# Kernel optimization log

Hardware: AMD Instinct MI355X
Metric: run time of the kernel (lower is better)

## Reference

```python
import jax, jax.numpy as jnp
import numpy as np

D_MODEL = 2048
D_FFN = 8192
RANK = 16
MOD_SCALE = 0.1
EPS = 1e-6


def setup_inputs() -> dict:
    key = jax.random.key(0)
    ks = jax.random.split(key, 8)
    B, S = 2, 2048
    init_scale = 0.01
    return {
        'hidden_states': jax.random.normal(ks[0], (B, S, D_MODEL), jnp.float32),
        'attn_output': jax.random.normal(ks[1], (B, S, D_MODEL), jnp.float32),
        'A': jax.random.normal(ks[2], (D_MODEL, RANK), jnp.float32) * (init_scale / np.sqrt(D_MODEL)),
        'Bmat': jax.random.normal(ks[3], (RANK, D_FFN), jnp.float32) * (init_scale / np.sqrt(RANK)),
        'W_in': jax.random.normal(ks[4], (D_FFN, D_MODEL), jnp.float32) * 0.02,  # gate_proj.weight
        'W_up': jax.random.normal(ks[5], (D_FFN, D_MODEL), jnp.float32) * 0.02,  # up_proj.weight
        'W_down': jax.random.normal(ks[6], (D_MODEL, D_FFN), jnp.float32) * 0.02,  # down_proj.weight
        'gamma': jnp.ones((D_MODEL,), jnp.float32),  # post_attention_layernorm (RMSNorm) weight
    }


def _rmsnorm(x, gamma):
    var = jnp.mean(x * x, axis=-1, keepdims=True)
    return x * jax.lax.rsqrt(var + EPS) * gamma


def reference(hidden_states, attn_output, A, Bmat, W_in, W_up, W_down, gamma):
    residual = hidden_states
    # Neuro-plastic modulation: [B,S,r]
    modulation = MOD_SCALE * jnp.tanh(jnp.einsum('bsd,dr->bsr', attn_output, A))
    # NPT applies post-attn norm to the residual (not residual+attn)
    h = _rmsnorm(residual, gamma)  # [B,S,d_model]
    # Fused per-token weight delta: delta_w^T @ h == B^T ((A^T h) * mod)
    hA = jnp.einsum('bsd,dr->bsr', h, A)  # [B,S,r]
    delta_out = jnp.einsum('bsr,rf->bsf', hA * modulation, Bmat)  # [B,S,d_ffn]
    gate = jax.nn.silu(jnp.einsum('bsd,fd->bsf', h, W_in) + delta_out)
    up = jnp.einsum('bsd,fd->bsf', h, W_up)
    out = jnp.einsum('bsf,df->bsd', gate * up, W_down)
    return residual + out
```

## Files before the change

### kernel.cpp

```cpp
#include <hip/hip_runtime.h>
#include <cstdint>
#include <cstddef>

#define D_MODEL 2048
#define D_FFN   8192
#define RANK    16
#define EPS     1e-6f
#define MOD_SCALE 0.1f

typedef float    f32x4 __attribute__((ext_vector_type(4)));
typedef _Float16 half8 __attribute__((ext_vector_type(8)));

__device__ __forceinline__ void async_load16(const void* g, void* l) {
  __builtin_amdgcn_global_load_lds(
      (const __attribute__((address_space(1))) uint32_t*)g,
      (__attribute__((address_space(3))) uint32_t*)l,
      16, 0, 0);
}

__device__ __forceinline__ void stage_round(const _Float16* __restrict__ g,
                                            size_t stride, _Float16* l, int tid) {
  const int row = tid >> 3;
  const int cs  = (tid & 7) ^ (row & 7);
  async_load16(g + (size_t)row * stride + (size_t)cs * 8, l + tid * 8);
}

__device__ __forceinline__ half8 frag64(const _Float16* base, int row, int ck) {
  return *(const half8*)&base[row * 64 + ((ck ^ (row & 7)) * 8)];
}

#define PRIO1() __builtin_amdgcn_s_setprio(1)
#define PRIO0() __builtin_amdgcn_s_setprio(0)
#define VMW(n)  asm volatile("s_waitcnt vmcnt(" #n ")" ::: "memory")
#define LKW(n)  asm volatile("s_waitcnt lgkmcnt(" #n ")" ::: "memory")
#define BARM()  asm volatile("s_barrier" ::: "memory")

__global__ __launch_bounds__(256) void convert3_f32_f16(
    const float* __restrict__ s0, const float* __restrict__ s1,
    const float* __restrict__ s2,
    _Float16* __restrict__ d0, _Float16* __restrict__ d1,
    _Float16* __restrict__ d2)
{
  const int w = blockIdx.x >> 13;
  const float*   s = (w == 0) ? s0 : (w == 1) ? s1 : s2;
  _Float16*      d = (w == 0) ? d0 : (w == 1) ? d1 : d2;
  size_t i = ((size_t)(blockIdx.x & 8191) * 256 + threadIdx.x) * 8;
  f32x4 a = *(const f32x4*)(s + i);
  f32x4 b = *(const f32x4*)(s + i + 4);
  half8 h;
  #pragma unroll
  for (int j = 0; j < 4; ++j) { h[j] = (_Float16)a[j]; h[4+j] = (_Float16)b[j]; }
  *(half8*)(d + i) = h;
}

__global__ __launch_bounds__(256) void convert_f32_f16(
    const float* __restrict__ s, _Float16* __restrict__ d)
{
  size_t i = ((size_t)blockIdx.x * 256 + threadIdx.x) * 8;
  f32x4 a = *(const f32x4*)(s + i);
  f32x4 b = *(const f32x4*)(s + i + 4);
  half8 h;
  #pragma unroll
  for (int j = 0; j < 4; ++j) { h[j] = (_Float16)a[j]; h[4+j] = (_Float16)b[j]; }
  *(half8*)(d + i) = h;
}

__global__ __launch_bounds__(256) void prep_kernel(
    const float* __restrict__ hs, const float* __restrict__ attn,
    const float* __restrict__ Amat, const float* __restrict__ gamma,
    _Float16* __restrict__ h16, float* __restrict__ cmat)
{
  const int token = blockIdx.x;
  const int tid   = threadIdx.x;
  const int lane  = tid & 63;
  const int wv    = tid >> 6;
  const size_t tb = (size_t)token * D_MODEL;
  const int base  = tid * 8;

  f32x4 x0 = *(const f32x4*)(hs + tb + base);
  f32x4 x1 = *(const f32x4*)(hs + tb + base + 4);
  f32x4 a0 = *(const f32x4*)(attn + tb + base);
  f32x4 a1 = *(const f32x4*)(attn + tb + base + 4);

  float ss = 0.f;
  #pragma unroll
  for (int j = 0; j < 4; ++j) ss += x0[j]*x0[j] + x1[j]*x1[j];
  #pragma unroll
  for (int off = 32; off > 0; off >>= 1) ss += __shfl_xor(ss, off, 64);

  __shared__ float red[4];
  __shared__ float redp[4][RANK];
  __shared__ float redh[4][RANK];
  if (lane == 0) red[wv] = ss;
  __syncthreads();
  const float tot = red[0] + red[1] + red[2] + red[3];
  const float rms = rsqrtf(tot * (1.0f / D_MODEL) + EPS);

  f32x4 g0 = *(const f32x4*)(gamma + base);
  f32x4 g1 = *(const f32x4*)(gamma + base + 4);
  float hv[8], av[8];
  #pragma unroll
  for (int j = 0; j < 4; ++j) {
    hv[j]   = x0[j] * rms * g0[j];
    hv[4+j] = x1[j] * rms * g1[j];
    av[j]   = a0[j];
    av[4+j] = a1[j];
  }
  half8 hh;
  #pragma unroll
  for (int j = 0; j < 8; ++j) hh[j] = (_Float16)hv[j];
  *(half8*)(h16 + tb + base) = hh;

  float pa[RANK], ph[RANK];
  #pragma unroll
  for (int r = 0; r < RANK; ++r) { pa[r] = 0.f; ph[r] = 0.f; }
  #pragma unroll
  for (int e = 0; e < 8; ++e) {
    const f32x4* Ar = (const f32x4*)(Amat + (size_t)(base + e) * RANK);
    #pragma unroll
    for (int q = 0; q < 4; ++q) {
      f32x4 ar = Ar[q];
      #pragma unroll
      for (int j = 0; j < 4; ++j) {
        pa[q*4+j] += av[e] * ar[j];
        ph[q*4+j] += hv[e] * ar[j];
      }
    }
  }
  #pragma unroll
  for (int r = 0; r < RANK; ++r) {
    #pragma unroll
    for (int off = 32; off > 0; off >>= 1) {
      pa[r] += __shfl_xor(pa[r], off, 64);
      ph[r] += __shfl_xor(ph[r], off, 64);
    }
  }
  if (lane == 0) {
    #pragma unroll
    for (int r = 0; r < RANK; ++r) { redp[wv][r] = pa[r]; redh[wv][r] = ph[r]; }
  }
  __syncthreads();
  if (tid < RANK) {
    float sp = redp[0][tid] + redp[1][tid] + redp[2][tid] + redp[3][tid];
    float sh = redh[0][tid] + redh[1][tid] + redh[2][tid] + redh[3][tid];
    cmat[(size_t)token * RANK + tid] = sh * (MOD_SCALE * tanhf(sp));
  }
}

__device__ __forceinline__ void rdA(half8 (&d)[4][2], const _Float16* Ab,
                                    int lr, int quad) {
  #pragma unroll
  for (int im = 0; im < 4; ++im)
    #pragma unroll
    for (int kk = 0; kk < 2; ++kk)
      d[im][kk] = frag64(Ab, im*16 + lr, kk*4 + quad);
}
__device__ __forceinline__ void rdB(half8 (&d)[2][2], const _Float16* Bb,
                                    int lr, int quad) {
  #pragma unroll
  for (int inn = 0; inn < 2; ++inn)
    #pragma unroll
    for (int kk = 0; kk < 2; ++kk)
      d[inn][kk] = frag64(Bb, inn*16 + lr, kk*4 + quad);
}
__device__ __forceinline__ void cluster(f32x4 (&acc)[8][2], int base,
                                        const half8 (&a)[4][2],
                                        const half8 (&b)[2][2]) {
  #pragma unroll
  for (int im = 0; im < 4; ++im)
    #pragma unroll
    for (int inn = 0; inn < 2; ++inn)
      #pragma unroll
      for (int kk = 0; kk < 2; ++kk)
        acc[base+im][inn] = __builtin_amdgcn_mfma_f32_16x16x32_f16(
            a[im][kk], b[inn][kk], acc[base+im][inn], 0, 0, 0);
}

#define BGOFF 16384
#define BUOFF 24576

__global__ __launch_bounds__(512, 2) void gemm_gateup(
    const _Float16* __restrict__ h16,
    const _Float16* __restrict__ Wg16, const _Float16* __restrict__ Wu16,
    const float* __restrict__ cmat, const float* __restrict__ Bmat,
    _Float16* __restrict__ tmat)
{
  __shared__ __align__(16) _Float16 lds[2][32768];

  const int tid  = threadIdx.x;
  const int lane = tid & 63;
  const int wv   = tid >> 6;
  const int lr   = lane & 15;
  const int quad = lane >> 4;
  const int qb   = (wv >> 2) * 2;
  const int e    = wv & 3;
  const int wm   = (wv >> 2) * 128;

  const int lin  = blockIdx.x;
  const int xcd  = lin & 7;
  const int r    = lin >> 3;
  const int gm0  = (xcd * 2 + (r & 1)) * 256;
  const int gn0  = (r >> 1) * 128;

  f32x4 accG[8][2], accU[8][2];
  #pragma unroll
  for (int i = 0; i < 8; ++i)
    #pragma unroll
    for (int j = 0; j < 2; ++j) {
      f32x4 z = {0.f, 0.f, 0.f, 0.f};
      accG[i][j] = z; accU[i][j] = z;
    }

#define STAE(b,t) do { \
    stage_round(h16 + (size_t)(gm0 +   0) * D_MODEL + (size_t)(t)*64, D_MODEL, &lds[b][0],     tid); \
    stage_round(h16 + (size_t)(gm0 + 128) * D_MODEL + (size_t)(t)*64, D_MODEL, &lds[b][8192],  tid); } while (0)
#define STAO(b,t) do { \
    stage_round(h16 + (size_t)(gm0 +  64) * D_MODEL + (size_t)(t)*64, D_MODEL, &lds[b][4096],  tid); \
    stage_round(h16 + (size_t)(gm0 + 192) * D_MODEL + (size_t)(t)*64, D_MODEL, &lds[b][12288], tid); } while (0)
#define STG(b,t) do { \
    stage_round(Wg16 + (size_t)(gn0 +  0) * D_MODEL + (size_t)(t)*64, D_MODEL, &lds[b][BGOFF],        tid); \
    stage_round(Wg16 + (size_t)(gn0 + 64) * D_MODEL + (size_t)(t)*64, D_MODEL, &lds[b][BGOFF + 4096], tid); } while (0)
#define STU(b,t) do { \
    stage_round(Wu16 + (size_t)(gn0 +  0) * D_MODEL + (size_t)(t)*64, D_MODEL, &lds[b][BUOFF],        tid); \
    stage_round(Wu16 + (size_t)(gn0 + 64) * D_MODEL + (size_t)(t)*64, D_MODEL, &lds[b][BUOFF + 4096], tid); } while (0)

#define PH4(BUF, S1, S2, S3, S4, W4)                                       \
  {                                                                        \
    const _Float16* A_  = &lds[BUF][0];                                    \
    const _Float16* Bg_ = &lds[BUF][BGOFF + e * 2048];                     \
    const _Float16* Bu_ = &lds[BUF][BUOFF + e * 2048];                     \
    half8 af[4][2], ao[4][2], bg[2][2], bu[2][2];                          \
    rdA(af, A_ + qb * 4096, lr, quad);                                     \
    rdB(bg, Bg_, lr, quad);                                                \
    S1; LKW(8);                                                            \
    BARM(); PRIO1(); cluster(accG, 0, af, bg); PRIO0(); BARM();            \
    rdB(bu, Bu_, lr, quad);                                                \
    S2;                                                                    \
    BARM(); PRIO1(); cluster(accU, 0, af, bu); PRIO0(); BARM();            \
    rdA(ao, A_ + (qb + 1) * 4096, lr, quad);                               \
    S3;                                                                    \
    BARM(); PRIO1(); cluster(accU, 4, ao, bu); PRIO0(); BARM();            \
    S4;                                                                    \
    BARM(); PRIO1(); cluster(accG, 4, ao, bg); PRIO0();                    \
    W4; BARM();                                                            \
  }

  STAE(0, 0); STAO(0, 0); STG(0, 0); STU(0, 0);
  STG(1, 1);  STU(1, 1);  STAE(1, 1);
  VMW(6); BARM();

  #pragma unroll 1
  for (int i = 0; i < 16; ++i) {
    const int t1 = 2*i + 1, t2 = 2*i + 2, t3 = 2*i + 3;
    const bool more = (i < 15);
    PH4(0,
        { STAO(1, t1); },
        { if (more) STG(0, t2); },
        { if (more) STU(0, t2); },
        { if (more) STAE(0, t2); },
        { if (more) { VMW(6); } else { VMW(0); } });
    PH4(1,
        { if (more) STAO(0, t2); },
        { if (more) STG(1, t3); },
        { if (more) STU(1, t3); },
        { if (more) STAE(1, t3); },
        { if (more) { VMW(6); } else { VMW(0); } });
  }

  __syncthreads();
  _Float16* l0 = &lds[0][0];
  for (int i = tid; i < 8192; i += 512) {
    int m = i >> 5, k = i & 31;
    l0[i] = (k < RANK) ? (_Float16)cmat[(size_t)(gm0 + m) * RANK + k] : (_Float16)0.f;
  }
  for (int i = tid; i < 4096; i += 512) {
    int f = i >> 5, k = i & 31;
    l0[8192 + i] = (k < RANK) ? (_Float16)Bmat[(size_t)k * D_FFN + gn0 + f] : (_Float16)0.f;
  }
  __syncthreads();
  #pragma unroll
  for (int ai = 0; ai < 8; ++ai) {
    half8 cf = *(const half8*)&l0[(wm + ai*16 + lr) * 32 + quad * 8];
    #pragma unroll
    for (int inn = 0; inn < 2; ++inn) {
      half8 bd = *(const half8*)&l0[8192 + (e*32 + inn*16 + lr) * 32 + quad * 8];
      accG[ai][inn] = __builtin_amdgcn_mfma_f32_16x16x32_f16(cf, bd, accG[ai][inn], 0, 0, 0);
    }
  }

  #pragma unroll
  for (int ai = 0; ai < 8; ++ai)
    #pragma unroll
    for (int inn = 0; inn < 2; ++inn) {
      const int grow = gm0 + wm + ai*16 + quad*4;
      const int gcol = gn0 + e*32 + inn*16 + lr;
      #pragma unroll
      for (int rr = 0; rr < 4; ++rr) {
        float g = accG[ai][inn][rr];
        float u = accU[ai][inn][rr];
        float s = g / (1.0f + __expf(-g));
        tmat[(size_t)(grow + rr) * D_FFN + gcol] = (_Float16)(s * u);
      }
    }
#undef STAE
#undef STAO
#undef STG
#undef STU
#undef PH4
}

__global__ __launch_bounds__(512, 2) void gemm_down(
    const _Float16* __restrict__ tmat, const _Float16* __restrict__ Wd16,
    const float* __restrict__ hs, float* __restrict__ out)
{
  __shared__ __align__(16) _Float16 lds[3][24576];

  const int tid  = threadIdx.x;
  const int lane = tid & 63;
  const int wv   = tid >> 6;
  const int lr   = lane & 15;
  const int quad = lane >> 4;
  const int qb   = (wv >> 2) * 2;
  const int e    = wv & 3;
  const int wm   = (wv >> 2) * 128;

  const int lin  = blockIdx.x;
  const int xcd  = lin & 7;
  const int r    = lin >> 3;
  const int gn0  = (xcd * 2 + (r & 1)) * 128;
  const int gm0  = (r >> 1) * 256;

  constexpr int NT = D_FFN / 64;

  f32x4 acc[8][2];
  #pragma unroll
  for (int i = 0; i < 8; ++i)
    #pragma unroll
    for (int j = 0; j < 2; ++j) {
      f32x4 z = {0.f, 0.f, 0.f, 0.f};
      acc[i][j] = z;
    }

#define DSTA(b,q,t) stage_round(tmat + (size_t)(gm0 + (q)*64) * D_FFN + (size_t)(t)*64, D_FFN, &lds[b][(q)*4096], tid)
#define DSTB(b,p,t) stage_round(Wd16 + (size_t)(gn0 + (p)*64) * D_FFN + (size_t)(t)*64, D_FFN, &lds[b][16384 + (p)*4096], tid)
#define DSTAGE_ALL(b,t) do { DSTA(b,0,t); DSTA(b,1,t); DSTA(b,2,t); DSTA(b,3,t); \
                             DSTB(b,0,t); DSTB(b,1,t); } while (0)

  DSTAGE_ALL(0, 0);
  DSTAGE_ALL(1, 1);
  VMW(6); BARM();

  int cur = 0;
  for (int t = 0; t < NT; ++t) {
    const _Float16* A = &lds[cur][0];
    const _Float16* B = &lds[cur][16384 + e * 2048];
    int nx2 = cur + 2; if (nx2 >= 3) nx2 -= 3;

    if (t + 2 < NT) DSTAGE_ALL(nx2, t + 2);

    half8 bf[2][2], af[4][2];
    #pragma unroll
    for (int inn = 0; inn < 2; ++inn)
      #pragma unroll
      for (int kk = 0; kk < 2; ++kk)
        bf[inn][kk] = frag64(B, inn*16 + lr, kk*4 + quad);
    #pragma unroll
    for (int im = 0; im < 4; ++im)
      #pragma unroll
      for (int kk = 0; kk < 2; ++kk)
        af[im][kk] = frag64(A + (qb + 0) * 4096, im*16 + lr, kk*4 + quad);

    PRIO1();
    #pragma unroll
    for (int im = 0; im < 4; ++im)
      #pragma unroll
      for (int inn = 0; inn < 2; ++inn)
        #pragma unroll
        for (int kk = 0; kk < 2; ++kk)
          acc[im][inn] = __builtin_amdgcn_mfma_f32_16x16x32_f16(af[im][kk], bf[inn][kk], acc[im][inn], 0, 0, 0);
    PRIO0();

    half8 ao[4][2];
    #pragma unroll
    for (int im = 0; im < 4; ++im)
      #pragma unroll
      for (int kk = 0; kk < 2; ++kk)
        ao[im][kk] = frag64(A + (qb + 1) * 4096, im*16 + lr, kk*4 + quad);

    PRIO1();
    #pragma unroll
    for (int im = 0; im < 4; ++im)
      #pragma unroll
      for (int inn = 0; inn < 2; ++inn)
        #pragma unroll
        for (int kk = 0; kk < 2; ++kk)
          acc[4+im][inn] = __builtin_amdgcn_mfma_f32_16x16x32_f16(ao[im][kk], bf[inn][kk], acc[4+im][inn], 0, 0, 0);
    PRIO0();

    if (t + 2 < NT) { VMW(6); } else { VMW(0); }
    BARM();

    cur += 1; if (cur >= 3) cur -= 3;
  }

  #pragma unroll
  for (int ai = 0; ai < 8; ++ai)
    #pragma unroll
    for (int inn = 0; inn < 2; ++inn) {
      const int grow = gm0 + wm + ai*16 + quad*4;
      const int gcol = gn0 + e*32 + inn*16 + lr;
      #pragma unroll
      for (int rr = 0; rr < 4; ++rr) {
        size_t o = (size_t)(grow + rr) * D_MODEL + gcol;
        out[o] = hs[o] + acc[ai][inn][rr];
      }
    }
#undef DSTA
#undef DSTB
#undef DSTAGE_ALL
}

extern "C" void kernel_launch(void* const* d_in, const int* in_sizes, int n_in,
                              void* d_out, int out_size, void* d_ws, size_t ws_size,
                              hipStream_t stream) {
  const float* hs    = (const float*)d_in[0];
  const float* attn  = (const float*)d_in[1];
  const float* Amat  = (const float*)d_in[2];
  const float* Bmat  = (const float*)d_in[3];
  const float* Wg    = (const float*)d_in[4];
  const float* Wu    = (const float*)d_in[5];
  const float* Wd    = (const float*)d_in[6];
  const float* gamma = (const float*)d_in[7];
  float* out = (float*)d_out;

  const int M = in_sizes[0] / D_MODEL;
  const size_t WD = (size_t)D_FFN * D_MODEL;

  char* ws = (char*)d_ws;
  _Float16* h16  = (_Float16*)ws;
  float*    cmat = (float*)(ws + (size_t)M * D_MODEL * 2);
  _Float16* tmat = (_Float16*)(ws + (size_t)M * D_MODEL * 2 + (size_t)M * RANK * 4);
  _Float16* wbuf = tmat + (size_t)M * D_FFN;
  _Float16* Wg16 = wbuf;
  _Float16* Wu16 = wbuf + WD;

  const size_t base_bytes = (size_t)M * D_MODEL * 2 + (size_t)M * RANK * 4
                          + (size_t)M * D_FFN * 2 + 2 * WD * 2;
  const bool sep_wd = (ws_size >= base_bytes + WD * 2);
  _Float16* Wd16 = sep_wd ? (wbuf + 2 * WD) : wbuf;

  const int convBlocks = (int)(WD / (256 * 8));

  prep_kernel<<<M, 256, 0, stream>>>(hs, attn, Amat, gamma, h16, cmat);
  if (sep_wd) {
    convert3_f32_f16<<<3 * convBlocks, 256, 0, stream>>>(Wg, Wu, Wd, Wg16, Wu16, Wd16);
    gemm_gateup<<<dim3((D_FFN / 128) * (M / 256)), 512, 0, stream>>>(h16, Wg16, Wu16, cmat, Bmat, tmat);
  } else {
    convert_f32_f16<<<convBlocks, 256, 0, stream>>>(Wg, Wg16);
    convert_f32_f16<<<convBlocks, 256, 0, stream>>>(Wu, Wu16);
    gemm_gateup<<<dim3((D_FFN / 128) * (M / 256)), 512, 0, stream>>>(h16, Wg16, Wu16, cmat, Bmat, tmat);
    convert_f32_f16<<<convBlocks, 256, 0, stream>>>(Wd, Wd16);
  }
  gemm_down<<<dim3((D_MODEL / 128) * (M / 256)), 512, 0, stream>>>(tmat, Wd16, hs, out);
}
```

Baseline: 743.0 us.

## Restructure gate/up and down GEMM pipelines with simpler double-buffered K-tiles

The gate/up GEMM's four-phase interleaved schedule, with its many barriers, is replaced by a simpler per-K-tile schedule. Each tile reads fragments in k-halves, issues the next tile's async loads between MFMA clusters, and ends with a full vmcnt(0) wait and one barrier. The down GEMM moves from a triple-buffered 8x2 per-wave tiling to double buffering with a 4x4 per-wave tile (qa/e split), which changes fragment reuse and LDS footprint. Fewer barriers and better A/B fragment reuse are the aim, but waiting for all loads each tile exposes more memory latency because prefetch depth drops to one tile.

```diff
diff --git a/kernel.cpp b/kernel.cpp
--- a/kernel.cpp
+++ b/kernel.cpp
@@ -32,7 +32,6 @@
 #define PRIO1() __builtin_amdgcn_s_setprio(1)
 #define PRIO0() __builtin_amdgcn_s_setprio(0)
 #define VMW(n)  asm volatile("s_waitcnt vmcnt(" #n ")" ::: "memory")
-#define LKW(n)  asm volatile("s_waitcnt lgkmcnt(" #n ")" ::: "memory")
 #define BARM()  asm volatile("s_barrier" ::: "memory")
 
 __global__ __launch_bounds__(256) void convert3_f32_f16(
@@ -147,33 +146,35 @@
   }
 }
 
-__device__ __forceinline__ void rdA(half8 (&d)[4][2], const _Float16* Ab,
-                                    int lr, int quad) {
+__device__ __forceinline__ void rdA4(half8 (&d)[4], const _Float16* Ab,
+                                     int lr, int ck) {
   #pragma unroll
   for (int im = 0; im < 4; ++im)
-    #pragma unroll
-    for (int kk = 0; kk < 2; ++kk)
-      d[im][kk] = frag64(Ab, im*16 + lr, kk*4 + quad);
-}
-__device__ __forceinline__ void rdB(half8 (&d)[2][2], const _Float16* Bb,
-                                    int lr, int quad) {
+    d[im] = frag64(Ab, im*16 + lr, ck);
+}
+__device__ __forceinline__ void rdB2(half8 (&d)[2], const _Float16* Bb,
+                                     int lr, int ck) {
   #pragma unroll
   for (int inn = 0; inn < 2; ++inn)
-    #pragma unroll
-    for (int kk = 0; kk < 2; ++kk)
-      d[inn][kk] = frag64(Bb, inn*16 + lr, kk*4 + quad);
-}
-__device__ __forceinline__ void cluster(f32x4 (&acc)[8][2], int base,
-                                        const half8 (&a)[4][2],
-                                        const half8 (&b)[2][2]) {
+    d[inn] = frag64(Bb, inn*16 + lr, ck);
+}
+__device__ __forceinline__ void mm8(f32x4 (&acc)[8][2], int mb,
+                                    const half8 (&a)[4], const half8 (&b)[2]) {
   #pragma unroll
   for (int im = 0; im < 4; ++im)
     #pragma unroll
     for (int inn = 0; inn < 2; ++inn)
-      #pragma unroll
-      for (int kk = 0; kk < 2; ++kk)
-        acc[base+im][inn] = __builtin_amdgcn_mfma_f32_16x16x32_f16(
-            a[im][kk], b[inn][kk], acc[base+im][inn], 0, 0, 0);
+      acc[mb+im][inn] = __builtin_amdgcn_mfma_f32_16x16x32_f16(
+          a[im], b[inn], acc[mb+im][inn], 0, 0, 0);
+}
+__device__ __forceinline__ void mm16(f32x4 (&acc)[4][4],
+                                     const half8 (&a)[4], const half8 (&b)[4]) {
+  #pragma unroll
+  for (int im = 0; im < 4; ++im)
+    #pragma unroll
+    for (int inn = 0; inn < 4; ++inn)
+      acc[im][inn] = __builtin_amdgcn_mfma_f32_16x16x32_f16(
+          a[im], b[inn], acc[im][inn], 0, 0, 0);
 }
 
 #define BGOFF 16384
@@ -224,47 +225,36 @@
     stage_round(Wu16 + (size_t)(gn0 +  0) * D_MODEL + (size_t)(t)*64, D_MODEL, &lds[b][BUOFF],        tid); \
     stage_round(Wu16 + (size_t)(gn0 + 64) * D_MODEL + (size_t)(t)*64, D_MODEL, &lds[b][BUOFF + 4096], tid); } while (0)
 
-#define PH4(BUF, S1, S2, S3, S4, W4)                                       \
+#define KTILE(BUF, SBUF, T1, DOSTG)                                        \
   {                                                                        \
     const _Float16* A_  = &lds[BUF][0];                                    \
     const _Float16* Bg_ = &lds[BUF][BGOFF + e * 2048];                     \
     const _Float16* Bu_ = &lds[BUF][BUOFF + e * 2048];                     \
-    half8 af[4][2], ao[4][2], bg[2][2], bu[2][2];                          \
-    rdA(af, A_ + qb * 4096, lr, quad);                                     \
-    rdB(bg, Bg_, lr, quad);                                                \
-    S1; LKW(8);                                                            \
-    BARM(); PRIO1(); cluster(accG, 0, af, bg); PRIO0(); BARM();            \
-    rdB(bu, Bu_, lr, quad);                                                \
-    S2;                                                                    \
-    BARM(); PRIO1(); cluster(accU, 0, af, bu); PRIO0(); BARM();            \
-    rdA(ao, A_ + (qb + 1) * 4096, lr, quad);                               \
-    S3;                                                                    \
-    BARM(); PRIO1(); cluster(accU, 4, ao, bu); PRIO0(); BARM();            \
-    S4;                                                                    \
-    BARM(); PRIO1(); cluster(accG, 4, ao, bg); PRIO0();                    \
-    W4; BARM();                                                            \
+    half8 a0[4], a1[4], a2[4], a3[4], bg0[2], bu0[2], bg1[2], bu1[2];      \
+    rdA4(a0, A_ + qb * 4096, lr, quad);                                    \
+    rdB2(bg0, Bg_, lr, quad);                                              \
+    rdB2(bu0, Bu_, lr, quad);                                              \
+    if (DOSTG) { STAE(SBUF, T1); STG(SBUF, T1); }                          \
+    rdA4(a1, A_ + (qb + 1) * 4096, lr, quad);                              \
+    PRIO1(); mm8(accG, 0, a0, bg0); mm8(accU, 0, a0, bu0); PRIO0();        \
+    if (DOSTG) { STAO(SBUF, T1); STU(SBUF, T1); }                          \
+    rdA4(a2, A_ + qb * 4096, lr, 4 + quad);                                \
+    rdB2(bg1, Bg_, lr, 4 + quad);                                          \
+    rdB2(bu1, Bu_, lr, 4 + quad);                                          \
+    PRIO1(); mm8(accG, 4, a1, bg0); mm8(accU, 4, a1, bu0); PRIO0();        \
+    rdA4(a3, A_ + (qb + 1) * 4096, lr, 4 + quad);                          \
+    PRIO1(); mm8(accG, 0, a2, bg1); mm8(accU, 0, a2, bu1); PRIO0();        \
+    PRIO1(); mm8(accG, 4, a3, bg1); mm8(accU, 4, a3, bu1); PRIO0();        \
+    VMW(0); BARM();                                                        \
   }
 
   STAE(0, 0); STAO(0, 0); STG(0, 0); STU(0, 0);
-  STG(1, 1);  STU(1, 1);  STAE(1, 1);
-  VMW(6); BARM();
+  VMW(0); BARM();
 
   #pragma unroll 1
   for (int i = 0; i < 16; ++i) {
-    const int t1 = 2*i + 1, t2 = 2*i + 2, t3 = 2*i + 3;
-    const bool more = (i < 15);
-    PH4(0,
-        { STAO(1, t1); },
-        { if (more) STG(0, t2); },
-        { if (more) STU(0, t2); },
-        { if (more) STAE(0, t2); },
-        { if (more) { VMW(6); } else { VMW(0); } });
-    PH4(1,
-        { if (more) STAO(0, t2); },
-        { if (more) STG(1, t3); },
-        { if (more) STU(1, t3); },
-        { if (more) STAE(1, t3); },
-        { if (more) { VMW(6); } else { VMW(0); } });
+    KTILE(0, 1, 2*i + 1, true);
+    KTILE(1, 0, 2*i + 2, (i < 15));
   }
 
   __syncthreads();
@@ -306,23 +296,22 @@
 #undef STAO
 #undef STG
 #undef STU
-#undef PH4
+#undef KTILE
 }
 
 __global__ __launch_bounds__(512, 2) void gemm_down(
     const _Float16* __restrict__ tmat, const _Float16* __restrict__ Wd16,
     const float* __restrict__ hs, float* __restrict__ out)
 {
-  __shared__ __align__(16) _Float16 lds[3][24576];
+  __shared__ __align__(16) _Float16 lds[2][24576];
 
   const int tid  = threadIdx.x;
   const int lane = tid & 63;
   const int wv   = tid >> 6;
   const int lr   = lane & 15;
   const int quad = lane >> 4;
-  const int qb   = (wv >> 2) * 2;
-  const int e    = wv & 3;
-  const int wm   = (wv >> 2) * 128;
+  const int qa   = wv >> 1;
+  const int e    = wv & 1;
 
   const int lin  = blockIdx.x;
   const int xcd  = lin & 7;
@@ -330,94 +319,58 @@
   const int gn0  = (xcd * 2 + (r & 1)) * 128;
   const int gm0  = (r >> 1) * 256;
 
-  constexpr int NT = D_FFN / 64;
-
-  f32x4 acc[8][2];
-  #pragma unroll
-  for (int i = 0; i < 8; ++i)
-    #pragma unroll
-    for (int j = 0; j < 2; ++j) {
+  f32x4 acc[4][4];
+  #pragma unroll
+  for (int i = 0; i < 4; ++i)
+    #pragma unroll
+    for (int j = 0; j < 4; ++j) {
       f32x4 z = {0.f, 0.f, 0.f, 0.f};
       acc[i][j] = z;
     }
 
 #define DSTA(b,q,t) stage_round(tmat + (size_t)(gm0 + (q)*64) * D_FFN + (size_t)(t)*64, D_FFN, &lds[b][(q)*4096], tid)
 #define DSTB(b,p,t) stage_round(Wd16 + (size_t)(gn0 + (p)*64) * D_FFN + (size_t)(t)*64, D_FFN, &lds[b][16384 + (p)*4096], tid)
-#define DSTAGE_ALL(b,t) do { DSTA(b,0,t); DSTA(b,1,t); DSTA(b,2,t); DSTA(b,3,t); \
-                             DSTB(b,0,t); DSTB(b,1,t); } while (0)
-
-  DSTAGE_ALL(0, 0);
-  DSTAGE_ALL(1, 1);
-  VMW(6); BARM();
-
-  int cur = 0;
-  for (int t = 0; t < NT; ++t) {
-    const _Float16* A = &lds[cur][0];
-    const _Float16* B = &lds[cur][16384 + e * 2048];
-    int nx2 = cur + 2; if (nx2 >= 3) nx2 -= 3;
-
-    if (t + 2 < NT) DSTAGE_ALL(nx2, t + 2);
-
-    half8 bf[2][2], af[4][2];
-    #pragma unroll
-    for (int inn = 0; inn < 2; ++inn)
-      #pragma unroll
-      for (int kk = 0; kk < 2; ++kk)
-        bf[inn][kk] = frag64(B, inn*16 + lr, kk*4 + quad);
-    #pragma unroll
-    for (int im = 0; im < 4; ++im)
-      #pragma unroll
-      for (int kk = 0; kk < 2; ++kk)
-        af[im][kk] = frag64(A + (qb + 0) * 4096, im*16 + lr, kk*4 + quad);
-
-    PRIO1();
-    #pragma unroll
-    for (int im = 0; im < 4; ++im)
-      #pragma unroll
-      for (int inn = 0; inn < 2; ++inn)
-        #pragma unroll
-        for (int kk = 0; kk < 2; ++kk)
-          acc[im][inn] = __builtin_amdgcn_mfma_f32_16x16x32_f16(af[im][kk], bf[inn][kk], acc[im][inn], 0, 0, 0);
-    PRIO0();
-
-    half8 ao[4][2];
-    #pragma unroll
-    for (int im = 0; im < 4; ++im)
-      #pragma unroll
-      for (int kk = 0; kk < 2; ++kk)
-        ao[im][kk] = frag64(A + (qb + 1) * 4096, im*16 + lr, kk*4 + quad);
-
-    PRIO1();
-    #pragma unroll
-    for (int im = 0; im < 4; ++im)
-      #pragma unroll
-      for (int inn = 0; inn < 2; ++inn)
-        #pragma unroll
-        for (int kk = 0; kk < 2; ++kk)
-          acc[4+im][inn] = __builtin_amdgcn_mfma_f32_16x16x32_f16(ao[im][kk], bf[inn][kk], acc[4+im][inn], 0, 0, 0);
-    PRIO0();
-
-    if (t + 2 < NT) { VMW(6); } else { VMW(0); }
-    BARM();
-
-    cur += 1; if (cur >= 3) cur -= 3;
-  }
-
-  #pragma unroll
-  for (int ai = 0; ai < 8; ++ai)
-    #pragma unroll
-    for (int inn = 0; inn < 2; ++inn) {
-      const int grow = gm0 + wm + ai*16 + quad*4;
-      const int gcol = gn0 + e*32 + inn*16 + lr;
+
+#define DKTILE(BUF, SBUF, T1, DOSTG)                                       \
+  {                                                                        \
+    const _Float16* A_ = &lds[BUF][qa * 4096];                             \
+    const _Float16* B_ = &lds[BUF][16384 + e * 4096];                      \
+    half8 a0[4], a1[4], b0[4], b1[4];                                      \
+    rdA4(a0, A_, lr, quad);                                                \
+    rdA4(b0, B_, lr, quad);                                                \
+    if (DOSTG) { DSTA(SBUF, 0, T1); DSTA(SBUF, 1, T1); DSTA(SBUF, 2, T1); }\
+    rdA4(a1, A_, lr, 4 + quad);                                            \
+    rdA4(b1, B_, lr, 4 + quad);                                            \
+    PRIO1(); mm16(acc, a0, b0); PRIO0();                                   \
+    if (DOSTG) { DSTA(SBUF, 3, T1); DSTB(SBUF, 0, T1); DSTB(SBUF, 1, T1); }\
+    PRIO1(); mm16(acc, a1, b1); PRIO0();                                   \
+    VMW(0); BARM();                                                        \
+  }
+
+  DSTA(0,0,0); DSTA(0,1,0); DSTA(0,2,0); DSTA(0,3,0); DSTB(0,0,0); DSTB(0,1,0);
+  VMW(0); BARM();
+
+  #pragma unroll 1
+  for (int i = 0; i < 64; ++i) {
+    DKTILE(0, 1, 2*i + 1, true);
+    DKTILE(1, 0, 2*i + 2, (i < 63));
+  }
+
+  #pragma unroll
+  for (int im = 0; im < 4; ++im)
+    #pragma unroll
+    for (int inn = 0; inn < 4; ++inn) {
+      const int grow = gm0 + qa*64 + im*16 + quad*4;
+      const int gcol = gn0 + e*64 + inn*16 + lr;
       #pragma unroll
       for (int rr = 0; rr < 4; ++rr) {
         size_t o = (size_t)(grow + rr) * D_MODEL + gcol;
-        out[o] = hs[o] + acc[ai][inn][rr];
+        out[o] = hs[o] + acc[im][inn][rr];
       }
     }
 #undef DSTA
 #undef DSTB
-#undef DSTAGE_ALL
+#undef DKTILE
 }
 
 extern "C" void kernel_launch(void* const* d_in, const int* in_sizes, int n_in,
```

Result: slower. 928.2 us (+24.9%).
